# Performance work log

Measured on AMD Instinct MI355X. Metric: run time of the kernel, lower is better.

Reference implementation:

```python
import jax, jax.numpy as jnp
import numpy as np

N = 100_000   # nodes
E = 1_600_000 # edges
IN = 128      # in_feats
H = 64        # h_feats
C = 16        # num_classes
L = 4         # num_layers
EPS = 1e-5    # BatchNorm eps


def setup_inputs() -> dict:
    key = jax.random.key(0)
    ks = jax.random.split(key, 16)
    w = lambda k, shape: jax.random.normal(k, shape, dtype=jnp.float32) * 0.02
    return {
        "features": jax.random.normal(ks[0], (N, IN), dtype=jnp.float32),
        "src": jax.random.randint(ks[1], (E,), 0, N),
        "dst": jax.random.randint(ks[2], (E,), 0, N),
        # RelationPatternEncoder: Linear(IN,IN/2) ReLU Linear(IN/2,IN/4) ReLU Linear(IN/4,IN)
        "enc_W1": w(ks[3], (IN, IN // 2)), "enc_b1": jnp.zeros((IN // 2,), jnp.float32),
        "enc_W2": w(ks[4], (IN // 2, IN // 4)), "enc_b2": jnp.zeros((IN // 4,), jnp.float32),
        "enc_W3": w(ks[5], (IN // 4, IN)), "enc_b3": jnp.zeros((IN,), jnp.float32),
        # attention gate: Linear(2H,H) ReLU Linear(H,1) Sigmoid
        "att_W1": w(ks[6], (2 * H, H)), "att_b1": jnp.zeros((H,), jnp.float32),
        "att_W2": w(ks[7], (H, 1)), "att_b2": jnp.zeros((1,), jnp.float32),
        # GraphConv weights: layer 0 (IN,H); layers 1..3 (H,H) stacked
        "W0": w(ks[8], (IN, H)), "b0": jnp.zeros((H,), jnp.float32),
        "W_rest": w(ks[9], (L - 1, H, H)), "b_rest": jnp.zeros((L - 1, H), jnp.float32),
        # BatchNorm affine params per layer
        "gamma": jnp.ones((L, H), jnp.float32), "beta": jnp.zeros((L, H), jnp.float32),
        # final classifier
        "fc_W": w(ks[10], (H, C)), "fc_b": jnp.zeros((C,), jnp.float32),
    }


def reference(features, src, dst, enc_W1, enc_b1, enc_W2, enc_b2, enc_W3, enc_b3,
              att_W1, att_b1, att_W2, att_b2, W0, b0, W_rest, b_rest,
              gamma, beta, fc_W, fc_b):
    n = features.shape[0]
    ones = jnp.ones(src.shape[0], jnp.float32)
    # degrees (DGL GraphConv norm='both' clamps degrees to min 1)
    out_deg = jnp.clip(jax.ops.segment_sum(ones, src, num_segments=n), 1.0)
    in_deg = jnp.clip(jax.ops.segment_sum(ones, dst, num_segments=n), 1.0)
    out_norm = out_deg ** -0.5  # [N]
    in_norm = in_deg ** -0.5    # [N]

    def graph_conv(h, W, b):
        # symmetric-normalized SpMM: D_in^{-1/2} A^T D_out^{-1/2} h, then linear
        hs = h * out_norm[:, None]
        agg = jax.ops.segment_sum(hs[src], dst, num_segments=n)  # [N,H]
        agg = agg * in_norm[:, None]
        return agg @ W + b

    def neighbor_mean(h):
        # update_all(copy_u, mean): mean over incoming edges, 0 for isolated nodes
        s = jax.ops.segment_sum(h[src], dst, num_segments=n)
        return s / in_deg[:, None]

    def batchnorm(x, g, bta):
        mu = x.mean(axis=0)
        var = x.var(axis=0)  # biased, as PyTorch uses in training normalization
        return (x - mu) * jax.lax.rsqrt(var + EPS) * g + bta

    # relation pattern encoder (last Linear has no activation)
    h = jax.nn.relu(features @ enc_W1 + enc_b1)
    h = jax.nn.relu(h @ enc_W2 + enc_b2)
    h = h @ enc_W3 + enc_b3  # [N, IN]

    for i in range(L):
        if i >= 1:
            nb = neighbor_mean(h)                       # [N,H]
            comb = jnp.concatenate([h, nb], axis=1)     # [N,2H]
            a = jax.nn.sigmoid(jax.nn.relu(comb @ att_W1 + att_b1) @ att_W2 + att_b2)  # [N,1]
            h = h + a * nb
        W, b = (W0, b0) if i == 0 else (W_rest[i - 1], b_rest[i - 1])
        h_new = batchnorm(graph_conv(h, W, b), gamma[i], beta[i])
        if i > 0:
            h_new = h_new + h  # residual
        h = jax.nn.relu(h_new)
        # dropout: identity in eval mode

    return h @ fc_W + fc_b  # [N, C]
```

## Files before the change

kernel.cpp:

```cpp
#include <hip/hip_runtime.h>
#include <hip/hip_bf16.h>
#include <math.h>


#define EPS_BN 1e-5f
#define GS_BLOCKS 2048

static inline int cdiv_i(int a, int b){ return (a + b - 1) / b; }

typedef __attribute__((ext_vector_type(8))) short bf16x8;
typedef __attribute__((ext_vector_type(4))) float f32x4;
typedef __attribute__((ext_vector_type(4))) unsigned short u16x4;

__device__ inline short f2bf(float f){
  unsigned int u = __builtin_bit_cast(unsigned int, f);
  u += 0x7FFFu + ((u >> 16) & 1u);
  return (short)(u >> 16);
}
__device__ inline float bf2f(unsigned short u){
  unsigned int x = ((unsigned int)u) << 16;
  return __builtin_bit_cast(float, x);
}

__device__ inline void pack_w_lds(const float* __restrict__ W, short* WP, int K, int N){
  int NF = N >> 4;
  int items = (K >> 5) * NF * 64;
  for (int i = threadIdx.x; i < items; i += 256){
    int c  = i & 15;
    int kg = (i >> 4) & 3;
    int t2 = i >> 6;
    int nf = t2 % NF, kstep = t2 / NF;
    short* d = &WP[((kstep * NF + nf) * 4 + kg) * 128 + c * 8];
#pragma unroll
    for (int j = 0; j < 8; ++j){
      int k = kstep * 32 + kg * 8 + j;
      d[j] = f2bf(W[(size_t)k * N + nf * 16 + c]);
    }
  }
}
__device__ inline bf16x8 wfrag(const short* WP, int NF, int kstep, int nf, int lgrp, int lrow){
  return *reinterpret_cast<const bf16x8*>(&WP[((kstep * NF + nf) * 4 + lgrp) * 128 + lrow * 8]);
}

__global__ void k_cnt2(const int* __restrict__ src, const int* __restrict__ dst,
                       float* __restrict__ outd, int* __restrict__ cnt,
                       int* __restrict__ rank, int E){
  int base = blockIdx.x * (blockDim.x * 4) + threadIdx.x;
#pragma unroll
  for (int j = 0; j < 4; ++j){
    int e = base + j * 256;
    if (e < E){
      atomicAdd(&outd[src[e]], 1.f);
      rank[e] = atomicAdd(&cnt[dst[e]], 1);
    }
  }
}

#define SCAN_B 256
__global__ void k_scan_a(const int* __restrict__ cnt, int* __restrict__ bsum,
                         float* __restrict__ outn, float* __restrict__ innorm,
                         float* __restrict__ invind, int n){
  __shared__ int sm[SCAN_B];
  int i = blockIdx.x * SCAN_B + threadIdx.x;
  int c = (i < n) ? cnt[i] : 0;
  if (i < n){
    float od = fmaxf(outn[i], 1.f);
    float id = fmaxf((float)c, 1.f);
    outn[i]   = rsqrtf(od);
    innorm[i] = rsqrtf(id);
    invind[i] = 1.f / id;
  }
  sm[threadIdx.x] = c;
  __syncthreads();
  for (int s = SCAN_B / 2; s; s >>= 1){
    if (threadIdx.x < s) sm[threadIdx.x] += sm[threadIdx.x + s];
    __syncthreads();
  }
  if (threadIdx.x == 0) bsum[blockIdx.x] = sm[0];
}

__global__ void k_scan_b(int* __restrict__ bsum, int nb, int* __restrict__ rowptr_n, int E){
  __shared__ int sm[512];
  int t = threadIdx.x;
  int orig = (t < nb) ? bsum[t] : 0;
  sm[t] = orig;
  __syncthreads();
  for (int off = 1; off < 512; off <<= 1){
    int v = (t >= off) ? sm[t - off] : 0;
    __syncthreads();
    sm[t] += v;
    __syncthreads();
  }
  if (t < nb) bsum[t] = sm[t] - orig;
  if (t == 0) *rowptr_n = E;
}

__global__ void k_scan_c(const int* __restrict__ cnt, const int* __restrict__ bsum,
                         int* __restrict__ rowptr, int n){
  __shared__ int sm[SCAN_B];
  int i = blockIdx.x * SCAN_B + threadIdx.x;
  int orig = (i < n) ? cnt[i] : 0;
  sm[threadIdx.x] = orig;
  __syncthreads();
  for (int off = 1; off < SCAN_B; off <<= 1){
    int v = (threadIdx.x >= off) ? sm[threadIdx.x - off] : 0;
    __syncthreads();
    sm[threadIdx.x] += v;
    __syncthreads();
  }
  if (i < n) rowptr[i] = sm[threadIdx.x] - orig + bsum[blockIdx.x];
}

__global__ void k_fill2(const int* __restrict__ src, const int* __restrict__ dst,
                        const int* __restrict__ rowptr, const int* __restrict__ rank,
                        int* __restrict__ csr, int E){
  int base = blockIdx.x * (blockDim.x * 4) + threadIdx.x;
#pragma unroll
  for (int j = 0; j < 4; ++j){
    int e = base + j * 256;
    if (e < E) csr[rowptr[dst[e]] + rank[e]] = src[e];
  }
}

__global__ __launch_bounds__(256) void k_enc(
    const float* __restrict__ features,
    const float* __restrict__ W1, const float* __restrict__ b1,
    const float* __restrict__ W2, const float* __restrict__ b2,
    const float* __restrict__ W3, const float* __restrict__ b3,
    const float* __restrict__ W0, const float* __restrict__ outnorm,
    unsigned short* __restrict__ hw_bf, int n)
{
  __shared__ short WP1[8192];
  __shared__ short WP2[2048];
  __shared__ short WP3[4096];
  __shared__ short stA[9216];
  __shared__ short st2[2560];

  const int tid = threadIdx.x, wave = tid >> 6, lane = tid & 63;
  const int lrow = lane & 15, lgrp = lane >> 4;
  const int row0 = blockIdx.x * 64;
  const int arow = row0 + wave * 16 + lrow;
  const bool rok = arow < n;

  pack_w_lds(W1, WP1, 128, 64);
  pack_w_lds(W2, WP2, 64, 32);
  pack_w_lds(W3, WP3, 32, 128);
  __syncthreads();

  {
    f32x4 acc[4] = {};
#pragma unroll
    for (int kstep = 0; kstep < 4; ++kstep){
      bf16x8 a;
      if (rok){
        const float* p = features + (size_t)arow * 128 + kstep * 32 + lgrp * 8;
        float4 v0 = *reinterpret_cast<const float4*>(p);
        float4 v1 = *reinterpret_cast<const float4*>(p + 4);
        a[0]=f2bf(v0.x); a[1]=f2bf(v0.y); a[2]=f2bf(v0.z); a[3]=f2bf(v0.w);
        a[4]=f2bf(v1.x); a[5]=f2bf(v1.y); a[6]=f2bf(v1.z); a[7]=f2bf(v1.w);
      } else {
#pragma unroll
        for (int j = 0; j < 8; ++j) a[j] = 0;
      }
#pragma unroll
      for (int nf = 0; nf < 4; ++nf)
        acc[nf] = __builtin_amdgcn_mfma_f32_16x16x32_bf16(a, wfrag(WP1,4,kstep,nf,lgrp,lrow), acc[nf], 0,0,0);
    }
#pragma unroll
    for (int nf = 0; nf < 4; ++nf){
      float bv = b1[nf * 16 + lrow];
#pragma unroll
      for (int r = 0; r < 4; ++r)
        stA[(wave*16 + lgrp*4 + r) * 72 + nf*16 + lrow] = f2bf(fmaxf(acc[nf][r] + bv, 0.f));
    }
  }
  __syncthreads();

  pack_w_lds(W0, WP1, 128, 64);

  {
    f32x4 acc[2] = {};
#pragma unroll
    for (int kstep = 0; kstep < 2; ++kstep){
      bf16x8 a = *reinterpret_cast<const bf16x8*>(&stA[(wave*16 + lrow) * 72 + kstep*32 + lgrp*8]);
#pragma unroll
      for (int nf = 0; nf < 2; ++nf)
        acc[nf] = __builtin_amdgcn_mfma_f32_16x16x32_bf16(a, wfrag(WP2,2,kstep,nf,lgrp,lrow), acc[nf], 0,0,0);
    }
#pragma unroll
    for (int nf = 0; nf < 2; ++nf){
      float bv = b2[nf * 16 + lrow];
#pragma unroll
      for (int r = 0; r < 4; ++r)
        st2[(wave*16 + lgrp*4 + r) * 40 + nf*16 + lrow] = f2bf(fmaxf(acc[nf][r] + bv, 0.f));
    }
  }
  __syncthreads();

  {
    f32x4 acc[8] = {};
    bf16x8 a = *reinterpret_cast<const bf16x8*>(&st2[(wave*16 + lrow) * 40 + lgrp*8]);
#pragma unroll
    for (int nf = 0; nf < 8; ++nf)
      acc[nf] = __builtin_amdgcn_mfma_f32_16x16x32_bf16(a, wfrag(WP3,8,0,nf,lgrp,lrow), acc[nf], 0,0,0);
    __syncthreads();
#pragma unroll
    for (int nf = 0; nf < 8; ++nf){
      float bv = b3[nf * 16 + lrow];
#pragma unroll
      for (int r = 0; r < 4; ++r)
        stA[(wave*16 + lgrp*4 + r) * 136 + nf*16 + lrow] = f2bf(acc[nf][r] + bv);
    }
  }
  __syncthreads();

  {
    const float rs = rok ? outnorm[arow] : 0.f;
    f32x4 acc[4] = {};
#pragma unroll
    for (int kstep = 0; kstep < 4; ++kstep){
      bf16x8 raw = *reinterpret_cast<const bf16x8*>(&stA[(wave*16 + lrow) * 136 + kstep*32 + lgrp*8]);
      bf16x8 a;
#pragma unroll
      for (int j = 0; j < 8; ++j) a[j] = f2bf(bf2f((unsigned short)raw[j]) * rs);
#pragma unroll
      for (int nf = 0; nf < 4; ++nf)
        acc[nf] = __builtin_amdgcn_mfma_f32_16x16x32_bf16(a, wfrag(WP1,4,kstep,nf,lgrp,lrow), acc[nf], 0,0,0);
    }
#pragma unroll
    for (int nf = 0; nf < 4; ++nf){
#pragma unroll
      for (int r = 0; r < 4; ++r){
        int orow = row0 + wave*16 + lgrp*4 + r;
        if (orow < n) hw_bf[(size_t)orow * 64 + nf*16 + lrow] = (unsigned short)f2bf(acc[nf][r]);
      }
    }
  }
}

__global__ __launch_bounds__(256) void k_attconv(
    float* __restrict__ h, const unsigned short* __restrict__ nb_bf,
    const float* __restrict__ invind, const float* __restrict__ outnorm,
    const float* __restrict__ W1, const float* __restrict__ b1,
    const float* __restrict__ W2, const float* __restrict__ b2,
    const float* __restrict__ Wi, unsigned short* __restrict__ hw_bf, int n)
{
  __shared__ short WPA[8192];
  __shared__ short WPC[4096];
  __shared__ short ht[64 * 72];

  const int tid = threadIdx.x, wave = tid >> 6, lane = tid & 63;
  const int lrow = lane & 15, lgrp = lane >> 4;
  const int row0 = blockIdx.x * 64;
  const int arow = row0 + wave * 16 + lrow;
  const bool rok = arow < n;

  pack_w_lds(W1, WPA, 128, 64);
  pack_w_lds(Wi, WPC, 64, 64);
  __syncthreads();

  const float iv = rok ? invind[arow] : 0.f;
  f32x4 acc[4];
#pragma unroll
  for (int nf = 0; nf < 4; ++nf) acc[nf] = (f32x4){0.f,0.f,0.f,0.f};

#pragma unroll
  for (int kstep = 0; kstep < 4; ++kstep){
    bf16x8 a;
    if (rok){
      if (kstep < 2){
        const float* p = h + (size_t)arow * 64 + kstep * 32 + lgrp * 8;
        float4 v0 = *reinterpret_cast<const float4*>(p);
        float4 v1 = *reinterpret_cast<const float4*>(p + 4);
        a[0]=f2bf(v0.x); a[1]=f2bf(v0.y); a[2]=f2bf(v0.z); a[3]=f2bf(v0.w);
        a[4]=f2bf(v1.x); a[5]=f2bf(v1.y); a[6]=f2bf(v1.z); a[7]=f2bf(v1.w);
      } else {
        const unsigned short* p = nb_bf + (size_t)arow * 64 + (kstep & 1) * 32 + lgrp * 8;
        bf16x8 raw = *reinterpret_cast<const bf16x8*>(p);
#pragma unroll
        for (int j = 0; j < 8; ++j) a[j] = f2bf(bf2f((unsigned short)raw[j]) * iv);
      }
    } else {
#pragma unroll
      for (int j = 0; j < 8; ++j) a[j] = 0;
    }
#pragma unroll
    for (int nf = 0; nf < 4; ++nf)
      acc[nf] = __builtin_amdgcn_mfma_f32_16x16x32_bf16(a, wfrag(WPA,4,kstep,nf,lgrp,lrow), acc[nf], 0,0,0);
  }

  const float w2l[4] = {W2[lrow], W2[16 + lrow], W2[32 + lrow], W2[48 + lrow]};
  const float b2v = b2[0];
#pragma unroll
  for (int r = 0; r < 4; ++r){
    int orow = row0 + wave*16 + lgrp*4 + r;
    float p = 0.f;
#pragma unroll
    for (int nf = 0; nf < 4; ++nf)
      p += fmaxf(acc[nf][r] + b1[nf * 16 + lrow], 0.f) * w2l[nf];
    p += __shfl_xor(p, 1); p += __shfl_xor(p, 2);
    p += __shfl_xor(p, 4); p += __shfl_xor(p, 8);
    short h0 = 0, h1v = 0, h2v = 0, h3v = 0;
    if (orow < n){
      float a = 1.f / (1.f + expf(-(p + b2v)));
      float ivr = invind[orow];
      const unsigned short* np = nb_bf + (size_t)orow * 64 + lrow * 4;
      float4 hv = *reinterpret_cast<float4*>(&h[(size_t)orow * 64 + lrow * 4]);
      hv.x += a * bf2f(np[0]) * ivr; hv.y += a * bf2f(np[1]) * ivr;
      hv.z += a * bf2f(np[2]) * ivr; hv.w += a * bf2f(np[3]) * ivr;
      *reinterpret_cast<float4*>(&h[(size_t)orow * 64 + lrow * 4]) = hv;
      h0 = f2bf(hv.x); h1v = f2bf(hv.y); h2v = f2bf(hv.z); h3v = f2bf(hv.w);
    }
    short* d = &ht[(wave*16 + lgrp*4 + r) * 72 + lrow * 4];
    d[0] = h0; d[1] = h1v; d[2] = h2v; d[3] = h3v;
  }
  __syncthreads();

  {
    const float rs = rok ? outnorm[arow] : 0.f;
    f32x4 cacc[4];
#pragma unroll
    for (int nf = 0; nf < 4; ++nf) cacc[nf] = (f32x4){0.f,0.f,0.f,0.f};
#pragma unroll
    for (int kstep = 0; kstep < 2; ++kstep){
      bf16x8 raw = *reinterpret_cast<const bf16x8*>(&ht[(wave*16 + lrow) * 72 + kstep*32 + lgrp*8]);
      bf16x8 a;
#pragma unroll
      for (int j = 0; j < 8; ++j) a[j] = f2bf(bf2f((unsigned short)raw[j]) * rs);
#pragma unroll
      for (int nf = 0; nf < 4; ++nf)
        cacc[nf] = __builtin_amdgcn_mfma_f32_16x16x32_bf16(a, wfrag(WPC,4,kstep,nf,lgrp,lrow), cacc[nf], 0,0,0);
    }
#pragma unroll
    for (int nf = 0; nf < 4; ++nf){
#pragma unroll
      for (int r = 0; r < 4; ++r){
        int orow = row0 + wave*16 + lgrp*4 + r;
        if (orow < n) hw_bf[(size_t)orow * 64 + nf*16 + lrow] = (unsigned short)f2bf(cacc[nf][r]);
      }
    }
  }
}

__global__ void k_gather_nb(const unsigned short* __restrict__ x,
                            const int* __restrict__ rowptr, const int* __restrict__ csr,
                            unsigned short* __restrict__ outv, int n){
  int node = blockIdx.x * 4 + (threadIdx.x >> 6);
  int f = threadIdx.x & 63;
  if (node >= n) return;
  int beg = rowptr[node], end = rowptr[node + 1];
  float a0 = 0.f, a1 = 0.f, a2 = 0.f, a3 = 0.f;
  int e = beg;
  for (; e + 3 < end; e += 4){
    int s0 = csr[e], s1 = csr[e+1], s2 = csr[e+2], s3 = csr[e+3];
    a0 += bf2f(x[(size_t)s0 * 64 + f]);
    a1 += bf2f(x[(size_t)s1 * 64 + f]);
    a2 += bf2f(x[(size_t)s2 * 64 + f]);
    a3 += bf2f(x[(size_t)s3 * 64 + f]);
  }
  for (; e < end; ++e) a0 += bf2f(x[(size_t)csr[e] * 64 + f]);
  outv[(size_t)node * 64 + f] = (unsigned short)f2bf((a0 + a1) + (a2 + a3));
}

__global__ __launch_bounds__(256) void k_gather_stats(
    const unsigned short* __restrict__ x, const int* __restrict__ rowptr,
    const int* __restrict__ csr, const float* __restrict__ innorm,
    const float* __restrict__ b, float* __restrict__ agg,
    float* __restrict__ p1, float* __restrict__ p2, int n){
  __shared__ float s1[4][64], s2[4][64];
  int g = threadIdx.x >> 6, f = threadIdx.x & 63;
  float bf = b[f];
  float z1 = 0.f, z2 = 0.f;
  for (int node = blockIdx.x * 4 + g; node < n; node += GS_BLOCKS * 4){
    int beg = rowptr[node], end = rowptr[node + 1];
    float a0 = 0.f, a1 = 0.f, a2 = 0.f, a3 = 0.f;
    int e = beg;
    for (; e + 3 < end; e += 4){
      int s0v = csr[e], s1v = csr[e+1], s2v = csr[e+2], s3v = csr[e+3];
      a0 += bf2f(x[(size_t)s0v * 64 + f]);
      a1 += bf2f(x[(size_t)s1v * 64 + f]);
      a2 += bf2f(x[(size_t)s2v * 64 + f]);
      a3 += bf2f(x[(size_t)s3v * 64 + f]);
    }
    for (; e < end; ++e) a0 += bf2f(x[(size_t)csr[e] * 64 + f]);
    float s = (a0 + a1) + (a2 + a3);
    agg[(size_t)node * 64 + f] = s;
    float z = s * innorm[node] + bf;
    z1 += z; z2 += z * z;
  }
  s1[g][f] = z1; s2[g][f] = z2;
  __syncthreads();
  if (threadIdx.x < 64){
    p1[(size_t)blockIdx.x * 64 + f] = s1[0][f] + s1[1][f] + s1[2][f] + s1[3][f];
    p2[(size_t)blockIdx.x * 64 + f] = s2[0][f] + s2[1][f] + s2[2][f] + s2[3][f];
  }
}

__global__ void k_bnred(const float* __restrict__ p1, const float* __restrict__ p2,
                        float* __restrict__ bnsum, float* __restrict__ bnsq){
  __shared__ float sm[256];
  int f = blockIdx.x & 63, stat = blockIdx.x >> 6;
  const float* p = stat ? p2 : p1;
  float a = 0.f;
  for (int i = threadIdx.x; i < GS_BLOCKS; i += 256) a += p[(size_t)i * 64 + f];
  sm[threadIdx.x] = a;
  __syncthreads();
  for (int s = 128; s; s >>= 1){
    if (threadIdx.x < s) sm[threadIdx.x] += sm[threadIdx.x + s];
    __syncthreads();
  }
  if (threadIdx.x == 0) (stat ? bnsq : bnsum)[f] = sm[0];
}

__global__ void k_post(const float* __restrict__ agg, const float* __restrict__ innorm,
                       const float* __restrict__ b, const float* __restrict__ bnsum,
                       const float* __restrict__ bnsq, const float* __restrict__ gamma,
                       const float* __restrict__ beta, float inv_n,
                       const float* __restrict__ hres,
                       float* __restrict__ hout, unsigned short* __restrict__ hbf, int n16){
  int i = blockIdx.x * blockDim.x + threadIdx.x;
  if (i >= n16) return;
  int row = i >> 4, fq = (i & 15) * 4;
  size_t o = (size_t)row * 64 + fq;
  float inn = innorm[row];
  float4 av = *reinterpret_cast<const float4*>(&agg[o]);
  float4 rv = hres ? *reinterpret_cast<const float4*>(&hres[o]) : (float4){0.f,0.f,0.f,0.f};
  float r[4]; float aa[4] = {av.x, av.y, av.z, av.w}; float rr[4] = {rv.x, rv.y, rv.z, rv.w};
#pragma unroll
  for (int j = 0; j < 4; ++j){
    int f = fq + j;
    float mu  = bnsum[f] * inv_n;
    float var = bnsq[f] * inv_n - mu * mu;
    float sc  = gamma[f] * rsqrtf(var + EPS_BN);
    float sh  = beta[f] - mu * sc;
    float z = aa[j] * inn + b[f];
    z = z * sc + sh + rr[j];
    r[j] = fmaxf(z, 0.f);
  }
  *reinterpret_cast<float4*>(&hout[o]) = (float4){r[0], r[1], r[2], r[3]};
  u16x4 hb;
#pragma unroll
  for (int j = 0; j < 4; ++j) hb[j] = (unsigned short)f2bf(r[j]);
  *reinterpret_cast<u16x4*>(&hbf[o]) = hb;
}

__global__ __launch_bounds__(256) void k_postfc(
    const float* __restrict__ agg, const float* __restrict__ innorm,
    const float* __restrict__ b, const float* __restrict__ bnsum,
    const float* __restrict__ bnsq, const float* __restrict__ gamma,
    const float* __restrict__ beta, float inv_n,
    const float* __restrict__ hres, const float* __restrict__ fcW,
    const float* __restrict__ fcb, float* __restrict__ out, int n)
{
  __shared__ short hb[64 * 72];
  __shared__ short WPF[1024];

  const int tid = threadIdx.x, wave = tid >> 6, lane = tid & 63;
  const int lrow = lane & 15, lgrp = lane >> 4;
  const int row0 = blockIdx.x * 64;

  pack_w_lds(fcW, WPF, 64, 16);

#pragma unroll
  for (int j = 0; j < 16; ++j){
    int idx = j * 256 + tid;
    int row = idx >> 6, f = idx & 63;
    int grow = row0 + row;
    float r = 0.f;
    if (grow < n){
      float mu  = bnsum[f] * inv_n;
      float var = bnsq[f] * inv_n - mu * mu;
      float sc  = gamma[f] * rsqrtf(var + EPS_BN);
      float sh  = beta[f] - mu * sc;
      float z = agg[(size_t)grow * 64 + f] * innorm[grow] + b[f];
      z = z * sc + sh + hres[(size_t)grow * 64 + f];
      r = fmaxf(z, 0.f);
    }
    hb[row * 72 + f] = f2bf(r);
  }
  __syncthreads();

  f32x4 acc = (f32x4){0.f,0.f,0.f,0.f};
#pragma unroll
  for (int kstep = 0; kstep < 2; ++kstep){
    bf16x8 a = *reinterpret_cast<const bf16x8*>(&hb[(wave*16 + lrow) * 72 + kstep*32 + lgrp*8]);
    acc = __builtin_amdgcn_mfma_f32_16x16x32_bf16(a, wfrag(WPF,1,kstep,0,lgrp,lrow), acc, 0,0,0);
  }
  float bv = fcb[lrow];
#pragma unroll
  for (int r = 0; r < 4; ++r){
    int orow = row0 + wave*16 + lgrp*4 + r;
    if (orow < n) out[(size_t)orow * 16 + lrow] = acc[r] + bv;
  }
}

extern "C" void kernel_launch(void* const* d_in, const int* in_sizes, int n_in,
                              void* d_out, int out_size, void* d_ws, size_t ws_size,
                              hipStream_t stream) {
  const float* features = (const float*)d_in[0];
  const int*   src      = (const int*)d_in[1];
  const int*   dst      = (const int*)d_in[2];
  const float* encW1 = (const float*)d_in[3];  const float* encb1 = (const float*)d_in[4];
  const float* encW2 = (const float*)d_in[5];  const float* encb2 = (const float*)d_in[6];
  const float* encW3 = (const float*)d_in[7];  const float* encb3 = (const float*)d_in[8];
  const float* attW1 = (const float*)d_in[9];  const float* attb1 = (const float*)d_in[10];
  const float* attW2 = (const float*)d_in[11]; const float* attb2 = (const float*)d_in[12];
  const float* W0    = (const float*)d_in[13]; const float* b0    = (const float*)d_in[14];
  const float* Wrest = (const float*)d_in[15]; const float* brest = (const float*)d_in[16];
  const float* gamma = (const float*)d_in[17]; const float* beta  = (const float*)d_in[18];
  const float* fcW   = (const float*)d_in[19]; const float* fcb   = (const float*)d_in[20];
  float* out = (float*)d_out;

  const int n = in_sizes[0] / 128;
  const int E = in_sizes[1];

  float* ws      = (float*)d_ws;
  float* agg     = ws;
  unsigned short* h_bf = (unsigned short*)(ws + (size_t)n * 64);
  float* p1      = ws + (size_t)n * 96;
  float* p2      = p1 + (size_t)GS_BLOCKS * 64;
  float* hbuf    = ws + (size_t)n * 128;
  float* nbhw    = hbuf + (size_t)n * 64;
  float* outnorm = nbhw + (size_t)n * 64;
  int*   cnt     = (int*)(outnorm + n);
  float* innorm  = (float*)(cnt + n);
  float* invind  = innorm + n;
  float* bnsum   = invind + n;
  float* bnsq    = bnsum + 256;
  int* rowptr = (int*)(bnsq + 256);
  int* csr    = rowptr + n + 1;
  int* bsum   = csr + E;
  int* rank = (int*)nbhw;
  unsigned short* nb_bf = (unsigned short*)nbhw;
  unsigned short* hw_bf = (unsigned short*)(nbhw + (size_t)n * 32);

  const int nt = cdiv_i(n, 64);
  const int nb = cdiv_i(n, SCAN_B);
  const float inv_n = 1.f / (float)n;

  hipMemsetAsync(outnorm, 0, 2 * (size_t)n * sizeof(float), stream);
  k_cnt2<<<cdiv_i(E, 1024), 256, 0, stream>>>(src, dst, outnorm, cnt, rank, E);
  k_scan_a<<<nb, SCAN_B, 0, stream>>>(cnt, bsum, outnorm, innorm, invind, n);
  k_scan_b<<<1, 512, 0, stream>>>(bsum, nb, rowptr + n, E);
  k_scan_c<<<nb, SCAN_B, 0, stream>>>(cnt, bsum, rowptr, n);
  k_fill2<<<cdiv_i(E, 1024), 256, 0, stream>>>(src, dst, rowptr, rank, csr, E);

  k_enc<<<nt, 256, 0, stream>>>(features, encW1, encb1, encW2, encb2, encW3, encb3,
                                W0, outnorm, hw_bf, n);
  k_gather_stats<<<GS_BLOCKS, 256, 0, stream>>>(hw_bf, rowptr, csr, innorm, b0, agg, p1, p2, n);
  k_bnred<<<128, 256, 0, stream>>>(p1, p2, bnsum, bnsq);
  k_post<<<cdiv_i(n * 16, 256), 256, 0, stream>>>(agg, innorm, b0, bnsum, bnsq, gamma, beta, inv_n,
                                                  nullptr, hbuf, h_bf, n * 16);

  for (int i = 1; i < 4; ++i){
    const float* Wi = Wrest + (size_t)(i - 1) * 64 * 64;
    const float* bi = brest + (size_t)(i - 1) * 64;
    k_gather_nb<<<cdiv_i(n, 4), 256, 0, stream>>>(h_bf, rowptr, csr, nb_bf, n);
    k_attconv<<<nt, 256, 0, stream>>>(hbuf, nb_bf, invind, outnorm,
                                      attW1, attb1, attW2, attb2, Wi, hw_bf, n);
    k_gather_stats<<<GS_BLOCKS, 256, 0, stream>>>(hw_bf, rowptr, csr, innorm, bi, agg, p1, p2, n);
    k_bnred<<<128, 256, 0, stream>>>(p1, p2, bnsum + i * 64, bnsq + i * 64);
    if (i < 3){
      k_post<<<cdiv_i(n * 16, 256), 256, 0, stream>>>(agg, innorm, bi, bnsum + i * 64, bnsq + i * 64,
                                                      gamma + i * 64, beta + i * 64, inv_n,
                                                      hbuf, hbuf, h_bf, n * 16);
    } else {
      k_postfc<<<nt, 256, 0, stream>>>(agg, innorm, bi, bnsum + i * 64, bnsq + i * 64,
                                       gamma + i * 64, beta + i * 64, inv_n,
                                       hbuf, fcW, fcb, out, n);
    }
  }
}
```

Baseline: 788.8 us.

## Fuse per-layer kernels into one cooperative persistent kernel with grid syncs

The five per-layer kernels (neighbor gather, attention+conv GEMM, gather with BN stats, BN reduction, post/fc) are merged into one cooperative kernel launched per layer, with grid.sync between phases. The grid is sized from occupancy, capped at 1024 blocks, and loops over tiles and nodes. The gather loops are unrolled to 8 accumulators, and attention weights are packed into LDS in two 64-row halves to shrink shared memory. This removes launch gaps and tail effects, at the cost of grid-wide barriers, repacking weights for every tile, and a grid that may be too small for the memory-bound gathers.

New measurement: 2.136 ms. +170.7%, slower.

```diff
diff --git a/kernel.cpp b/kernel.cpp
--- a/kernel.cpp
+++ b/kernel.cpp
@@ -1,10 +1,13 @@
 #include <hip/hip_runtime.h>
 #include <hip/hip_bf16.h>
+#include <hip/hip_cooperative_groups.h>
 #include <math.h>
 
 
 #define EPS_BN 1e-5f
 #define GS_BLOCKS 2048
+
+namespace cg = cooperative_groups;
 
 static inline int cdiv_i(int a, int b){ return (a + b - 1) / b; }
 
@@ -236,130 +239,6 @@
       }
     }
   }
-}
-
-__global__ __launch_bounds__(256) void k_attconv(
-    float* __restrict__ h, const unsigned short* __restrict__ nb_bf,
-    const float* __restrict__ invind, const float* __restrict__ outnorm,
-    const float* __restrict__ W1, const float* __restrict__ b1,
-    const float* __restrict__ W2, const float* __restrict__ b2,
-    const float* __restrict__ Wi, unsigned short* __restrict__ hw_bf, int n)
-{
-  __shared__ short WPA[8192];
-  __shared__ short WPC[4096];
-  __shared__ short ht[64 * 72];
-
-  const int tid = threadIdx.x, wave = tid >> 6, lane = tid & 63;
-  const int lrow = lane & 15, lgrp = lane >> 4;
-  const int row0 = blockIdx.x * 64;
-  const int arow = row0 + wave * 16 + lrow;
-  const bool rok = arow < n;
-
-  pack_w_lds(W1, WPA, 128, 64);
-  pack_w_lds(Wi, WPC, 64, 64);
-  __syncthreads();
-
-  const float iv = rok ? invind[arow] : 0.f;
-  f32x4 acc[4];
-#pragma unroll
-  for (int nf = 0; nf < 4; ++nf) acc[nf] = (f32x4){0.f,0.f,0.f,0.f};
-
-#pragma unroll
-  for (int kstep = 0; kstep < 4; ++kstep){
-    bf16x8 a;
-    if (rok){
-      if (kstep < 2){
-        const float* p = h + (size_t)arow * 64 + kstep * 32 + lgrp * 8;
-        float4 v0 = *reinterpret_cast<const float4*>(p);
-        float4 v1 = *reinterpret_cast<const float4*>(p + 4);
-        a[0]=f2bf(v0.x); a[1]=f2bf(v0.y); a[2]=f2bf(v0.z); a[3]=f2bf(v0.w);
-        a[4]=f2bf(v1.x); a[5]=f2bf(v1.y); a[6]=f2bf(v1.z); a[7]=f2bf(v1.w);
-      } else {
-        const unsigned short* p = nb_bf + (size_t)arow * 64 + (kstep & 1) * 32 + lgrp * 8;
-        bf16x8 raw = *reinterpret_cast<const bf16x8*>(p);
-#pragma unroll
-        for (int j = 0; j < 8; ++j) a[j] = f2bf(bf2f((unsigned short)raw[j]) * iv);
-      }
-    } else {
-#pragma unroll
-      for (int j = 0; j < 8; ++j) a[j] = 0;
-    }
-#pragma unroll
-    for (int nf = 0; nf < 4; ++nf)
-      acc[nf] = __builtin_amdgcn_mfma_f32_16x16x32_bf16(a, wfrag(WPA,4,kstep,nf,lgrp,lrow), acc[nf], 0,0,0);
-  }
-
-  const float w2l[4] = {W2[lrow], W2[16 + lrow], W2[32 + lrow], W2[48 + lrow]};
-  const float b2v = b2[0];
-#pragma unroll
-  for (int r = 0; r < 4; ++r){
-    int orow = row0 + wave*16 + lgrp*4 + r;
-    float p = 0.f;
-#pragma unroll
-    for (int nf = 0; nf < 4; ++nf)
-      p += fmaxf(acc[nf][r] + b1[nf * 16 + lrow], 0.f) * w2l[nf];
-    p += __shfl_xor(p, 1); p += __shfl_xor(p, 2);
-    p += __shfl_xor(p, 4); p += __shfl_xor(p, 8);
-    short h0 = 0, h1v = 0, h2v = 0, h3v = 0;
-    if (orow < n){
-      float a = 1.f / (1.f + expf(-(p + b2v)));
-      float ivr = invind[orow];
-      const unsigned short* np = nb_bf + (size_t)orow * 64 + lrow * 4;
-      float4 hv = *reinterpret_cast<float4*>(&h[(size_t)orow * 64 + lrow * 4]);
-      hv.x += a * bf2f(np[0]) * ivr; hv.y += a * bf2f(np[1]) * ivr;
-      hv.z += a * bf2f(np[2]) * ivr; hv.w += a * bf2f(np[3]) * ivr;
-      *reinterpret_cast<float4*>(&h[(size_t)orow * 64 + lrow * 4]) = hv;
-      h0 = f2bf(hv.x); h1v = f2bf(hv.y); h2v = f2bf(hv.z); h3v = f2bf(hv.w);
-    }
-    short* d = &ht[(wave*16 + lgrp*4 + r) * 72 + lrow * 4];
-    d[0] = h0; d[1] = h1v; d[2] = h2v; d[3] = h3v;
-  }
-  __syncthreads();
-
-  {
-    const float rs = rok ? outnorm[arow] : 0.f;
-    f32x4 cacc[4];
-#pragma unroll
-    for (int nf = 0; nf < 4; ++nf) cacc[nf] = (f32x4){0.f,0.f,0.f,0.f};
-#pragma unroll
-    for (int kstep = 0; kstep < 2; ++kstep){
-      bf16x8 raw = *reinterpret_cast<const bf16x8*>(&ht[(wave*16 + lrow) * 72 + kstep*32 + lgrp*8]);
-      bf16x8 a;
-#pragma unroll
-      for (int j = 0; j < 8; ++j) a[j] = f2bf(bf2f((unsigned short)raw[j]) * rs);
-#pragma unroll
-      for (int nf = 0; nf < 4; ++nf)
-        cacc[nf] = __builtin_amdgcn_mfma_f32_16x16x32_bf16(a, wfrag(WPC,4,kstep,nf,lgrp,lrow), cacc[nf], 0,0,0);
-    }
-#pragma unroll
-    for (int nf = 0; nf < 4; ++nf){
-#pragma unroll
-      for (int r = 0; r < 4; ++r){
-        int orow = row0 + wave*16 + lgrp*4 + r;
-        if (orow < n) hw_bf[(size_t)orow * 64 + nf*16 + lrow] = (unsigned short)f2bf(cacc[nf][r]);
-      }
-    }
-  }
-}
-
-__global__ void k_gather_nb(const unsigned short* __restrict__ x,
-                            const int* __restrict__ rowptr, const int* __restrict__ csr,
-                            unsigned short* __restrict__ outv, int n){
-  int node = blockIdx.x * 4 + (threadIdx.x >> 6);
-  int f = threadIdx.x & 63;
-  if (node >= n) return;
-  int beg = rowptr[node], end = rowptr[node + 1];
-  float a0 = 0.f, a1 = 0.f, a2 = 0.f, a3 = 0.f;
-  int e = beg;
-  for (; e + 3 < end; e += 4){
-    int s0 = csr[e], s1 = csr[e+1], s2 = csr[e+2], s3 = csr[e+3];
-    a0 += bf2f(x[(size_t)s0 * 64 + f]);
-    a1 += bf2f(x[(size_t)s1 * 64 + f]);
-    a2 += bf2f(x[(size_t)s2 * 64 + f]);
-    a3 += bf2f(x[(size_t)s3 * 64 + f]);
-  }
-  for (; e < end; ++e) a0 += bf2f(x[(size_t)csr[e] * 64 + f]);
-  outv[(size_t)node * 64 + f] = (unsigned short)f2bf((a0 + a1) + (a2 + a3));
 }
 
 __global__ __launch_bounds__(256) void k_gather_stats(
@@ -444,53 +323,270 @@
   *reinterpret_cast<u16x4*>(&hbf[o]) = hb;
 }
 
-__global__ __launch_bounds__(256) void k_postfc(
-    const float* __restrict__ agg, const float* __restrict__ innorm,
-    const float* __restrict__ b, const float* __restrict__ bnsum,
-    const float* __restrict__ bnsq, const float* __restrict__ gamma,
-    const float* __restrict__ beta, float inv_n,
-    const float* __restrict__ hres, const float* __restrict__ fcW,
-    const float* __restrict__ fcb, float* __restrict__ out, int n)
-{
-  __shared__ short hb[64 * 72];
-  __shared__ short WPF[1024];
+struct KL {
+  float* h; unsigned short* h_bf; unsigned short* nb_bf; unsigned short* hw_bf;
+  float* agg; float* p1; float* p2; float* bnsum; float* bnsq;
+  const float* invind; const float* innorm; const float* outnorm;
+  const int* rowptr; const int* csr;
+  const float* W1; const float* b1; const float* W2; const float* b2;
+  const float* Wi; const float* bi; const float* gamma; const float* beta;
+  const float* fcW; const float* fcb; float* outp;
+  float inv_n; int n; int last;
+};
+
+__global__ __launch_bounds__(256, 4) void k_layer(KL A){
+  cg::grid_group grid = cg::this_grid();
+  __shared__ __align__(16) short WP[4096];
+  __shared__ __align__(16) short ht[64 * 72];
+  __shared__ float sred[256];
 
   const int tid = threadIdx.x, wave = tid >> 6, lane = tid & 63;
   const int lrow = lane & 15, lgrp = lane >> 4;
-  const int row0 = blockIdx.x * 64;
-
-  pack_w_lds(fcW, WPF, 64, 16);
-
-#pragma unroll
-  for (int j = 0; j < 16; ++j){
-    int idx = j * 256 + tid;
-    int row = idx >> 6, f = idx & 63;
-    int grow = row0 + row;
-    float r = 0.f;
-    if (grow < n){
-      float mu  = bnsum[f] * inv_n;
-      float var = bnsq[f] * inv_n - mu * mu;
-      float sc  = gamma[f] * rsqrtf(var + EPS_BN);
-      float sh  = beta[f] - mu * sc;
-      float z = agg[(size_t)grow * 64 + f] * innorm[grow] + b[f];
-      z = z * sc + sh + hres[(size_t)grow * 64 + f];
-      r = fmaxf(z, 0.f);
-    }
-    hb[row * 72 + f] = f2bf(r);
-  }
-  __syncthreads();
-
-  f32x4 acc = (f32x4){0.f,0.f,0.f,0.f};
-#pragma unroll
-  for (int kstep = 0; kstep < 2; ++kstep){
-    bf16x8 a = *reinterpret_cast<const bf16x8*>(&hb[(wave*16 + lrow) * 72 + kstep*32 + lgrp*8]);
-    acc = __builtin_amdgcn_mfma_f32_16x16x32_bf16(a, wfrag(WPF,1,kstep,0,lgrp,lrow), acc, 0,0,0);
-  }
-  float bv = fcb[lrow];
-#pragma unroll
-  for (int r = 0; r < 4; ++r){
-    int orow = row0 + wave*16 + lgrp*4 + r;
-    if (orow < n) out[(size_t)orow * 16 + lrow] = acc[r] + bv;
+  const int G = gridDim.x;
+  const int n = A.n;
+  const int nt = (n + 63) >> 6;
+
+  {
+    int g = wave, f = lane;
+    for (int node = blockIdx.x * 4 + g; node < n; node += G * 4){
+      int beg = A.rowptr[node], end = A.rowptr[node + 1];
+      float a0=0.f,a1=0.f,a2=0.f,a3=0.f,a4=0.f,a5=0.f,a6=0.f,a7=0.f;
+      int e = beg;
+      for (; e + 7 < end; e += 8){
+        a0 += bf2f(A.h_bf[(size_t)A.csr[e  ] * 64 + f]);
+        a1 += bf2f(A.h_bf[(size_t)A.csr[e+1] * 64 + f]);
+        a2 += bf2f(A.h_bf[(size_t)A.csr[e+2] * 64 + f]);
+        a3 += bf2f(A.h_bf[(size_t)A.csr[e+3] * 64 + f]);
+        a4 += bf2f(A.h_bf[(size_t)A.csr[e+4] * 64 + f]);
+        a5 += bf2f(A.h_bf[(size_t)A.csr[e+5] * 64 + f]);
+        a6 += bf2f(A.h_bf[(size_t)A.csr[e+6] * 64 + f]);
+        a7 += bf2f(A.h_bf[(size_t)A.csr[e+7] * 64 + f]);
+      }
+      for (; e < end; ++e) a0 += bf2f(A.h_bf[(size_t)A.csr[e] * 64 + f]);
+      float s = ((a0+a1)+(a2+a3)) + ((a4+a5)+(a6+a7));
+      A.nb_bf[(size_t)node * 64 + f] = (unsigned short)f2bf(s);
+    }
+  }
+  grid.sync();
+
+  for (int t = blockIdx.x; t < nt; t += G){
+    const int row0 = t * 64;
+    const int arow = row0 + wave * 16 + lrow;
+    const bool rok = arow < n;
+
+    __syncthreads();
+    pack_w_lds(A.W1, WP, 64, 64);
+    __syncthreads();
+
+    f32x4 acc[4];
+#pragma unroll
+    for (int nf = 0; nf < 4; ++nf) acc[nf] = (f32x4){0.f,0.f,0.f,0.f};
+#pragma unroll
+    for (int kstep = 0; kstep < 2; ++kstep){
+      bf16x8 a;
+      if (rok){
+        const float* p = A.h + (size_t)arow * 64 + kstep * 32 + lgrp * 8;
+        float4 v0 = *reinterpret_cast<const float4*>(p);
+        float4 v1 = *reinterpret_cast<const float4*>(p + 4);
+        a[0]=f2bf(v0.x); a[1]=f2bf(v0.y); a[2]=f2bf(v0.z); a[3]=f2bf(v0.w);
+        a[4]=f2bf(v1.x); a[5]=f2bf(v1.y); a[6]=f2bf(v1.z); a[7]=f2bf(v1.w);
+      } else {
+#pragma unroll
+        for (int j = 0; j < 8; ++j) a[j] = 0;
+      }
+#pragma unroll
+      for (int nf = 0; nf < 4; ++nf)
+        acc[nf] = __builtin_amdgcn_mfma_f32_16x16x32_bf16(a, wfrag(WP,4,kstep,nf,lgrp,lrow), acc[nf], 0,0,0);
+    }
+    __syncthreads();
+    pack_w_lds(A.W1 + 64 * 64, WP, 64, 64);
+    __syncthreads();
+    const float iv = rok ? A.invind[arow] : 0.f;
+#pragma unroll
+    for (int kstep = 0; kstep < 2; ++kstep){
+      bf16x8 a;
+      if (rok){
+        bf16x8 raw = *reinterpret_cast<const bf16x8*>(
+            A.nb_bf + (size_t)arow * 64 + kstep * 32 + lgrp * 8);
+#pragma unroll
+        for (int j = 0; j < 8; ++j) a[j] = f2bf(bf2f((unsigned short)raw[j]) * iv);
+      } else {
+#pragma unroll
+        for (int j = 0; j < 8; ++j) a[j] = 0;
+      }
+#pragma unroll
+      for (int nf = 0; nf < 4; ++nf)
+        acc[nf] = __builtin_amdgcn_mfma_f32_16x16x32_bf16(a, wfrag(WP,4,kstep,nf,lgrp,lrow), acc[nf], 0,0,0);
+    }
+
+    const float w2l[4] = {A.W2[lrow], A.W2[16 + lrow], A.W2[32 + lrow], A.W2[48 + lrow]};
+    const float b2v = A.b2[0];
+#pragma unroll
+    for (int r = 0; r < 4; ++r){
+      int orow = row0 + wave*16 + lgrp*4 + r;
+      float p = 0.f;
+#pragma unroll
+      for (int nf = 0; nf < 4; ++nf)
+        p += fmaxf(acc[nf][r] + A.b1[nf * 16 + lrow], 0.f) * w2l[nf];
+      p += __shfl_xor(p, 1); p += __shfl_xor(p, 2);
+      p += __shfl_xor(p, 4); p += __shfl_xor(p, 8);
+      short h0 = 0, h1v = 0, h2v = 0, h3v = 0;
+      if (orow < n){
+        float a = 1.f / (1.f + expf(-(p + b2v)));
+        float ivr = A.invind[orow];
+        const unsigned short* np = A.nb_bf + (size_t)orow * 64 + lrow * 4;
+        float4 hv = *reinterpret_cast<float4*>(&A.h[(size_t)orow * 64 + lrow * 4]);
+        hv.x += a * bf2f(np[0]) * ivr; hv.y += a * bf2f(np[1]) * ivr;
+        hv.z += a * bf2f(np[2]) * ivr; hv.w += a * bf2f(np[3]) * ivr;
+        *reinterpret_cast<float4*>(&A.h[(size_t)orow * 64 + lrow * 4]) = hv;
+        h0 = f2bf(hv.x); h1v = f2bf(hv.y); h2v = f2bf(hv.z); h3v = f2bf(hv.w);
+      }
+      short* d = &ht[(wave*16 + lgrp*4 + r) * 72 + lrow * 4];
+      d[0] = h0; d[1] = h1v; d[2] = h2v; d[3] = h3v;
+    }
+    __syncthreads();
+    pack_w_lds(A.Wi, WP, 64, 64);
+    __syncthreads();
+
+    const float rs = rok ? A.outnorm[arow] : 0.f;
+    f32x4 cacc[4];
+#pragma unroll
+    for (int nf = 0; nf < 4; ++nf) cacc[nf] = (f32x4){0.f,0.f,0.f,0.f};
+#pragma unroll
+    for (int kstep = 0; kstep < 2; ++kstep){
+      bf16x8 raw = *reinterpret_cast<const bf16x8*>(&ht[(wave*16 + lrow) * 72 + kstep*32 + lgrp*8]);
+      bf16x8 a;
+#pragma unroll
+      for (int j = 0; j < 8; ++j) a[j] = f2bf(bf2f((unsigned short)raw[j]) * rs);
+#pragma unroll
+      for (int nf = 0; nf < 4; ++nf)
+        cacc[nf] = __builtin_amdgcn_mfma_f32_16x16x32_bf16(a, wfrag(WP,4,kstep,nf,lgrp,lrow), cacc[nf], 0,0,0);
+    }
+#pragma unroll
+    for (int nf = 0; nf < 4; ++nf){
+#pragma unroll
+      for (int r = 0; r < 4; ++r){
+        int orow = row0 + wave*16 + lgrp*4 + r;
+        if (orow < n) A.hw_bf[(size_t)orow * 64 + nf*16 + lrow] = (unsigned short)f2bf(cacc[nf][r]);
+      }
+    }
+  }
+  grid.sync();
+
+  {
+    int g = wave, f = lane;
+    float bf = A.bi[f];
+    float z1 = 0.f, z2 = 0.f;
+    for (int node = blockIdx.x * 4 + g; node < n; node += G * 4){
+      int beg = A.rowptr[node], end = A.rowptr[node + 1];
+      float a0=0.f,a1=0.f,a2=0.f,a3=0.f,a4=0.f,a5=0.f,a6=0.f,a7=0.f;
+      int e = beg;
+      for (; e + 7 < end; e += 8){
+        a0 += bf2f(A.hw_bf[(size_t)A.csr[e  ] * 64 + f]);
+        a1 += bf2f(A.hw_bf[(size_t)A.csr[e+1] * 64 + f]);
+        a2 += bf2f(A.hw_bf[(size_t)A.csr[e+2] * 64 + f]);
+        a3 += bf2f(A.hw_bf[(size_t)A.csr[e+3] * 64 + f]);
+        a4 += bf2f(A.hw_bf[(size_t)A.csr[e+4] * 64 + f]);
+        a5 += bf2f(A.hw_bf[(size_t)A.csr[e+5] * 64 + f]);
+        a6 += bf2f(A.hw_bf[(size_t)A.csr[e+6] * 64 + f]);
+        a7 += bf2f(A.hw_bf[(size_t)A.csr[e+7] * 64 + f]);
+      }
+      for (; e < end; ++e) a0 += bf2f(A.hw_bf[(size_t)A.csr[e] * 64 + f]);
+      float s = ((a0+a1)+(a2+a3)) + ((a4+a5)+(a6+a7));
+      A.agg[(size_t)node * 64 + f] = s;
+      float z = s * A.innorm[node] + bf;
+      z1 += z; z2 += z * z;
+    }
+    float* s1 = (float*)ht;
+    float* s2 = s1 + 256;
+    __syncthreads();
+    s1[g * 64 + f] = z1; s2[g * 64 + f] = z2;
+    __syncthreads();
+    if (tid < 64){
+      A.p1[(size_t)blockIdx.x * 64 + tid] = s1[tid] + s1[64+tid] + s1[128+tid] + s1[192+tid];
+      A.p2[(size_t)blockIdx.x * 64 + tid] = s2[tid] + s2[64+tid] + s2[128+tid] + s2[192+tid];
+    }
+  }
+  grid.sync();
+
+  if (blockIdx.x < 128){
+    int f = blockIdx.x & 63, stat = blockIdx.x >> 6;
+    const float* p = stat ? A.p2 : A.p1;
+    float a = 0.f;
+    for (int i = tid; i < G; i += 256) a += p[(size_t)i * 64 + f];
+    sred[tid] = a;
+    __syncthreads();
+    for (int s = 128; s; s >>= 1){
+      if (tid < s) sred[tid] += sred[tid + s];
+      __syncthreads();
+    }
+    if (tid == 0) (stat ? A.bnsq : A.bnsum)[f] = sred[0];
+  }
+  grid.sync();
+
+  if (!A.last){
+    int n16 = n * 16;
+    for (int i = blockIdx.x * 256 + tid; i < n16; i += G * 256){
+      int row = i >> 4, fq = (i & 15) * 4;
+      size_t o = (size_t)row * 64 + fq;
+      float inn = A.innorm[row];
+      float4 av = *reinterpret_cast<const float4*>(&A.agg[o]);
+      float4 rv = *reinterpret_cast<const float4*>(&A.h[o]);
+      float r[4]; float aa[4] = {av.x, av.y, av.z, av.w}; float rr[4] = {rv.x, rv.y, rv.z, rv.w};
+#pragma unroll
+      for (int j = 0; j < 4; ++j){
+        int f = fq + j;
+        float mu  = A.bnsum[f] * A.inv_n;
+        float var = A.bnsq[f] * A.inv_n - mu * mu;
+        float sc  = A.gamma[f] * rsqrtf(var + EPS_BN);
+        float sh  = A.beta[f] - mu * sc;
+        float z = aa[j] * inn + A.bi[f];
+        z = z * sc + sh + rr[j];
+        r[j] = fmaxf(z, 0.f);
+      }
+      *reinterpret_cast<float4*>(&A.h[o]) = (float4){r[0], r[1], r[2], r[3]};
+      u16x4 hb;
+#pragma unroll
+      for (int j = 0; j < 4; ++j) hb[j] = (unsigned short)f2bf(r[j]);
+      *reinterpret_cast<u16x4*>(&A.h_bf[o]) = hb;
+    }
+  } else {
+    for (int t = blockIdx.x; t < nt; t += G){
+      const int row0 = t * 64;
+      __syncthreads();
+      pack_w_lds(A.fcW, WP, 64, 16);
+#pragma unroll
+      for (int j = 0; j < 16; ++j){
+        int idx = j * 256 + tid;
+        int row = idx >> 6, f = idx & 63;
+        int grow = row0 + row;
+        float r = 0.f;
+        if (grow < n){
+          float mu  = A.bnsum[f] * A.inv_n;
+          float var = A.bnsq[f] * A.inv_n - mu * mu;
+          float sc  = A.gamma[f] * rsqrtf(var + EPS_BN);
+          float sh  = A.beta[f] - mu * sc;
+          float z = A.agg[(size_t)grow * 64 + f] * A.innorm[grow] + A.bi[f];
+          z = z * sc + sh + A.h[(size_t)grow * 64 + f];
+          r = fmaxf(z, 0.f);
+        }
+        ht[row * 72 + f] = f2bf(r);
+      }
+      __syncthreads();
+      f32x4 acc = (f32x4){0.f,0.f,0.f,0.f};
+#pragma unroll
+      for (int kstep = 0; kstep < 2; ++kstep){
+        bf16x8 a = *reinterpret_cast<const bf16x8*>(&ht[(wave*16 + lrow) * 72 + kstep*32 + lgrp*8]);
+        acc = __builtin_amdgcn_mfma_f32_16x16x32_bf16(a, wfrag(WP,1,kstep,0,lgrp,lrow), acc, 0,0,0);
+      }
+      float bv = A.fcb[lrow];
+#pragma unroll
+      for (int r = 0; r < 4; ++r){
+        int orow = row0 + wave*16 + lgrp*4 + r;
+        if (orow < n) A.outp[(size_t)orow * 16 + lrow] = acc[r] + bv;
+      }
+      __syncthreads();
+    }
   }
 }
 
@@ -538,6 +634,12 @@
   const int nb = cdiv_i(n, SCAN_B);
   const float inv_n = 1.f / (float)n;
 
+  int bpc = 0;
+  hipOccupancyMaxActiveBlocksPerMultiprocessor(&bpc, (const void*)k_layer, 256, 0);
+  if (bpc < 1) bpc = 1;
+  int G = bpc * 256;
+  if (G > 1024) G = 1024;
+
   hipMemsetAsync(outnorm, 0, 2 * (size_t)n * sizeof(float), stream);
   k_cnt2<<<cdiv_i(E, 1024), 256, 0, stream>>>(src, dst, outnorm, cnt, rank, E);
   k_scan_a<<<nb, SCAN_B, 0, stream>>>(cnt, bsum, outnorm, innorm, invind, n);
@@ -553,21 +655,19 @@
                                                   nullptr, hbuf, h_bf, n * 16);
 
   for (int i = 1; i < 4; ++i){
-    const float* Wi = Wrest + (size_t)(i - 1) * 64 * 64;
-    const float* bi = brest + (size_t)(i - 1) * 64;
-    k_gather_nb<<<cdiv_i(n, 4), 256, 0, stream>>>(h_bf, rowptr, csr, nb_bf, n);
-    k_attconv<<<nt, 256, 0, stream>>>(hbuf, nb_bf, invind, outnorm,
-                                      attW1, attb1, attW2, attb2, Wi, hw_bf, n);
-    k_gather_stats<<<GS_BLOCKS, 256, 0, stream>>>(hw_bf, rowptr, csr, innorm, bi, agg, p1, p2, n);
-    k_bnred<<<128, 256, 0, stream>>>(p1, p2, bnsum + i * 64, bnsq + i * 64);
-    if (i < 3){
-      k_post<<<cdiv_i(n * 16, 256), 256, 0, stream>>>(agg, innorm, bi, bnsum + i * 64, bnsq + i * 64,
-                                                      gamma + i * 64, beta + i * 64, inv_n,
-                                                      hbuf, hbuf, h_bf, n * 16);
-    } else {
-      k_postfc<<<nt, 256, 0, stream>>>(agg, innorm, bi, bnsum + i * 64, bnsq + i * 64,
-                                       gamma + i * 64, beta + i * 64, inv_n,
-                                       hbuf, fcW, fcb, out, n);
-    }
-  }
-}
+    KL a;
+    a.h = hbuf; a.h_bf = h_bf; a.nb_bf = nb_bf; a.hw_bf = hw_bf;
+    a.agg = agg; a.p1 = p1; a.p2 = p2;
+    a.bnsum = bnsum + i * 64; a.bnsq = bnsq + i * 64;
+    a.invind = invind; a.innorm = innorm; a.outnorm = outnorm;
+    a.rowptr = rowptr; a.csr = csr;
+    a.W1 = attW1; a.b1 = attb1; a.W2 = attW2; a.b2 = attb2;
+    a.Wi = Wrest + (size_t)(i - 1) * 64 * 64;
+    a.bi = brest + (size_t)(i - 1) * 64;
+    a.gamma = gamma + i * 64; a.beta = beta + i * 64;
+    a.fcW = fcW; a.fcb = fcb; a.outp = out;
+    a.inv_n = inv_n; a.n = n; a.last = (i == 3) ? 1 : 0;
+    void* kargs[] = { (void*)&a };
+    hipLaunchCooperativeKernel((const void*)k_layer, dim3(G), dim3(256), kargs, 0, stream);
+  }
+}
```
